# Performance work log

Measured on AMD Instinct MI355X. Metric: run time of the kernel, lower is better.

## Reference

```python
import jax, jax.numpy as jnp
import numpy as np

B, D, N, L, H, T = 256, 768, 256, 2, 8, 20
HD = D // H

def _ln(x, g, b):
    m = x.mean(-1, keepdims=True)
    v = ((x - m) ** 2).mean(-1, keepdims=True)
    return (x - m) / jnp.sqrt(v + 1e-5) * g + b

def setup_inputs() -> dict:
    key = jax.random.key(0)
    ks = jax.random.split(key, 8)
    kk = jax.random.split(ks[7], 10)
    def w(k, shape):
        return jax.random.normal(k, shape, jnp.float32) * 0.02
    return {
        'feats': jax.random.normal(ks[0], (B, D, N), jnp.float32),
        'past': jax.random.normal(ks[1], (B, 16, 6), jnp.float32),
        'w_qinit': w(ks[2], (121, D)), 'b_qinit': jnp.zeros((D,), jnp.float32),
        'pos_enc': w(ks[3], (1, N, D)),
        'w_pp': w(ks[4], (2, D)), 'b_pp': jnp.zeros((D,), jnp.float32),
        'g_pp': jnp.ones((D,), jnp.float32), 'be_pp': jnp.zeros((D,), jnp.float32),
        'time_emb': w(ks[5], (T, D)),
        'Wq': w(kk[0], (L, D, D)), 'bq': jnp.zeros((L, D), jnp.float32),
        'Wk': w(kk[1], (L, D, D)), 'bk': jnp.zeros((L, D), jnp.float32),
        'Wv': w(kk[2], (L, D, D)), 'bv': jnp.zeros((L, D), jnp.float32),
        'Wo': w(kk[3], (L, D, D)), 'bo': jnp.zeros((L, D), jnp.float32),
        'ln1_g': jnp.ones((L, D), jnp.float32), 'ln1_b': jnp.zeros((L, D), jnp.float32),
        'W1': w(kk[4], (L, D, 4 * D)), 'b1': jnp.zeros((L, 4 * D), jnp.float32),
        'W2': w(kk[5], (L, 4 * D, D)), 'b2': jnp.zeros((L, D), jnp.float32),
        'ln2_g': jnp.ones((L, D), jnp.float32), 'ln2_b': jnp.zeros((L, D), jnp.float32),
        'w_dec1': w(kk[6], (D, D)), 'b_dec1': jnp.zeros((D,), jnp.float32),
        'w_dec2': w(kk[7], (D, 2)), 'b_dec2': jnp.zeros((2,), jnp.float32),
        'intent': jax.random.randint(ks[6], (B,), 0, 3),
    }

def reference(feats, past, w_qinit, b_qinit, pos_enc, w_pp, b_pp, g_pp, be_pp,
              time_emb, Wq, bq, Wk, bk, Wv, bv, Wo, bo, ln1_g, ln1_b,
              W1, b1, W2, b2, ln2_g, ln2_b, w_dec1, b_dec1, w_dec2, b_dec2, intent):
    # tokens: [B, N, D]
    tokens = jnp.transpose(feats, (0, 2, 1)) + pos_enc
    onehot = jax.nn.one_hot(jnp.clip(intent - 1, 0, 2), 3, dtype=tokens.dtype)
    past_flat = past.reshape(B, -1)
    pad = jnp.zeros((B, 22), tokens.dtype)
    context = jnp.concatenate([onehot, past_flat, pad], axis=1) @ w_qinit + b_qinit  # [B, D]
    # precompute cross-attention K/V once per layer (tokens are constant across steps)
    Kh = (jnp.einsum('bnd,lde->lbne', tokens, Wk) + bk[:, None, None, :]).reshape(L, B, N, H, HD)
    Vh = (jnp.einsum('bnd,lde->lbne', tokens, Wv) + bv[:, None, None, :]).reshape(L, B, N, H, HD)
    scale = 1.0 / np.sqrt(HD)

    def step(carry, te):
        ctx, cp = carry
        pq = jax.nn.relu(_ln(cp @ w_pp + b_pp, g_pp, be_pp))
        x = (ctx + pq + te)[:, None, :]  # [B, 1, D]
        for l in range(L):
            q = (_ln(x, ln1_g[l], ln1_b[l]) @ Wq[l] + bq[l]).reshape(B, 1, H, HD)
            s = jnp.einsum('bqhd,bnhd->bhqn', q, Kh[l]) * scale
            a = jax.nn.softmax(s, axis=-1)
            o = jnp.einsum('bhqn,bnhd->bqhd', a, Vh[l]).reshape(B, 1, D) @ Wo[l] + bo[l]
            x = x + o
            h = jax.nn.gelu(_ln(x, ln2_g[l], ln2_b[l]) @ W1[l] + b1[l], approximate=False) @ W2[l] + b2[l]
            x = x + h
        ctx = x[:, 0]
        delta = jax.nn.gelu(ctx @ w_dec1 + b_dec1, approximate=False) @ w_dec2 + b_dec2
        cp = cp + delta
        return (ctx, cp), cp

    init = (context, past[:, -1, 0:2])
    _, ys = jax.lax.scan(step, init, time_emb)  # ys: [T, B, 2]
    return jnp.transpose(ys, (1, 0, 2))
```

## Files before the change

kernel.cpp:

```cpp
#include <hip/hip_runtime.h>
#include <hip/hip_bf16.h>
#include <math.h>

#define B_ 256
#define D_ 768
#define N_ 256
#define L_ 2
#define H_ 8
#define T_ 20
#define HD_ 96
#define D4_ 3072

typedef float f32x4v __attribute__((ext_vector_type(4)));
typedef __bf16 bf16x8v __attribute__((ext_vector_type(8)));

union V16 { uint4 u; bf16x8v v; };

__device__ __forceinline__ ushort f2b(float f) {
    union { float f; unsigned u; } x{f};
    unsigned r = x.u + 0x7fffu + ((x.u >> 16) & 1u);
    return (ushort)(r >> 16);
}
__device__ __forceinline__ float b2f(ushort s) {
    union { unsigned u; float f; } x{(unsigned)s << 16};
    return x.f;
}
__device__ __forceinline__ float gelu_f(float v) {
    return 0.5f * v * (1.0f + erff(v * 0.7071067811865476f));
}
__device__ __forceinline__ float dot8(const float* __restrict__ xp, uint4 u) {
    return xp[0] * b2f((ushort)(u.x & 0xffffu)) + xp[1] * b2f((ushort)(u.x >> 16))
         + xp[2] * b2f((ushort)(u.y & 0xffffu)) + xp[3] * b2f((ushort)(u.y >> 16))
         + xp[4] * b2f((ushort)(u.z & 0xffffu)) + xp[5] * b2f((ushort)(u.z >> 16))
         + xp[6] * b2f((ushort)(u.w & 0xffffu)) + xp[7] * b2f((ushort)(u.w >> 16));
}
__device__ __forceinline__ float blockSum(float v, float* red, int tid) {
    for (int off = 32; off; off >>= 1) v += __shfl_down(v, off, 64);
    int w = tid >> 6, lane = tid & 63;
    if (lane == 0) red[w] = v;
    __syncthreads();
    float r = red[0] + red[1] + red[2] + red[3];
    __syncthreads();
    return r;
}
__device__ __forceinline__ void gl_lds16(const ushort* g, ushort* l) {
    __builtin_amdgcn_global_load_lds((const __attribute__((address_space(1))) unsigned int*)g,
                                     (__attribute__((address_space(3))) unsigned int*)l,
                                     16, 0, 0);
}

__global__ __launch_bounds__(256) void context_kernel(const float* __restrict__ past,
                                                      const float* __restrict__ w_qinit,
                                                      const float* __restrict__ b_qinit,
                                                      const int* __restrict__ intent,
                                                      const float* __restrict__ w_pp,
                                                      const float* __restrict__ b_pp,
                                                      const float* __restrict__ g_pp,
                                                      const float* __restrict__ be_pp,
                                                      const float* __restrict__ te0,
                                                      float* __restrict__ x,
                                                      float* __restrict__ cp) {
    int b = blockIdx.x, tid = threadIdx.x;
    __shared__ float ps[96];
    __shared__ int oidx;
    __shared__ float red[4];
    if (tid < 96) ps[tid] = past[b * 96 + tid];
    if (tid == 0) {
        int iv = intent[b] - 1;
        oidx = iv < 0 ? 0 : (iv > 2 ? 2 : iv);
    }
    __syncthreads();
    float ctx[3];
    #pragma unroll
    for (int r = 0; r < 3; ++r) {
        int d = tid + r * 256;
        float acc = w_qinit[oidx * D_ + d] + b_qinit[d];
        #pragma unroll 8
        for (int p = 0; p < 96; ++p) acc += ps[p] * w_qinit[(3 + p) * D_ + d];
        ctx[r] = acc;
    }
    float c0 = ps[90], c1 = ps[91];
    if (tid == 0) { cp[b * 2] = c0; cp[b * 2 + 1] = c1; }
    float t[3];
    float s = 0, ss = 0;
    #pragma unroll
    for (int r = 0; r < 3; ++r) {
        int d = tid + r * 256;
        t[r] = c0 * w_pp[d] + c1 * w_pp[D_ + d] + b_pp[d];
        s += t[r]; ss += t[r] * t[r];
    }
    s = blockSum(s, red, tid);
    ss = blockSum(ss, red, tid);
    float mean = s * (1.0f / D_);
    float var = ss * (1.0f / D_) - mean * mean;
    float rinv = rsqrtf(var + 1e-5f);
    #pragma unroll
    for (int r = 0; r < 3; ++r) {
        int d = tid + r * 256;
        float pq = fmaxf((t[r] - mean) * rinv * g_pp[d] + be_pp[d], 0.0f);
        x[b * D_ + d] = ctx[r] + pq + te0[d];
    }
}

__global__ __launch_bounds__(256) void token_prep(const float* __restrict__ feats,
                                                  const float* __restrict__ pos_enc,
                                                  ushort* __restrict__ tokens) {
    int b = blockIdx.z;
    int d0 = blockIdx.x * 64, n0 = blockIdx.y * 64;
    __shared__ float tile[64][65];
    int tid = threadIdx.x;
    int nl = tid & 63, dl0 = tid >> 6;
    const float* fb = feats + ((size_t)b * D_ + d0) * N_ + n0;
    #pragma unroll
    for (int i = 0; i < 16; ++i) {
        int dl = dl0 + i * 4;
        tile[dl][nl] = fb[(size_t)dl * N_ + nl];
    }
    __syncthreads();
    int dq = (tid & 15) * 4;
    int ng = tid >> 4;
    #pragma unroll
    for (int i = 0; i < 4; ++i) {
        int nl2 = ng + i * 16;
        int n = n0 + nl2;
        float4 p = *(const float4*)(pos_enc + (size_t)n * D_ + d0 + dq);
        ushort4 o;
        o.x = f2b(tile[dq + 0][nl2] + p.x);
        o.y = f2b(tile[dq + 1][nl2] + p.y);
        o.z = f2b(tile[dq + 2][nl2] + p.z);
        o.w = f2b(tile[dq + 3][nl2] + p.w);
        *(ushort4*)&tokens[((size_t)b * N_ + n) * D_ + d0 + dq] = o;
    }
}

__global__ __launch_bounds__(256) void transpose_w(const float* __restrict__ W,
                                                   ushort* __restrict__ out,
                                                   const float* __restrict__ scale,
                                                   int K, int N) {
    __shared__ float t[32][33];
    int k0 = blockIdx.y * 32, n0 = blockIdx.x * 32;
    int tx = threadIdx.x & 31, ty = threadIdx.x >> 5;
    #pragma unroll
    for (int i = 0; i < 4; ++i)
        t[ty + i * 8][tx] = W[(size_t)(k0 + ty + i * 8) * N + n0 + tx];
    __syncthreads();
    #pragma unroll
    for (int i = 0; i < 4; ++i) {
        int n = n0 + ty + i * 8, k = k0 + tx;
        float v = t[tx][ty + i * 8];
        if (scale) v *= scale[k];
        out[(size_t)n * K + k] = f2b(v);
    }
}

__global__ __launch_bounds__(256) void bias_eff_kernel(const float* __restrict__ W,
                                                       const float* __restrict__ bias,
                                                       const float* __restrict__ lb,
                                                       float* __restrict__ be, int Nc) {
    int n = blockIdx.x * 256 + threadIdx.x;
    float a = bias[n];
    for (int k = 0; k < D_; ++k) a += lb[k] * W[(size_t)k * Nc + n];
    be[n] = a;
}

__global__ void kvbias_prep(const float* __restrict__ bk, const float* __restrict__ bv,
                            float* __restrict__ bc) {
    int i = blockIdx.x * 256 + threadIdx.x;
    int mi = i / D_, c = i % D_;
    int l = mi >> 1;
    bc[i] = (mi & 1 ? bv : bk)[l * D_ + c];
}

__global__ __launch_bounds__(256) void kv_gemm_mfma(const ushort* __restrict__ tokens,
                                                    const ushort* __restrict__ Wkvt,
                                                    const float* __restrict__ bias_kv,
                                                    ushort* __restrict__ Kt,
                                                    ushort* __restrict__ Vt) {
    int e0 = blockIdx.x * 128;
    int mi = e0 / D_;
    int ein = e0 % D_;
    int l = mi >> 1, isV = mi & 1;
    int m0 = blockIdx.y * 128;
    int b = m0 >> 8, ntok0 = m0 & 255;
    __shared__ __align__(16) ushort smem[17408];
    int tid = threadIdx.x;
    int w = tid >> 6, lane = tid & 63, quad = lane >> 4, l16 = lane & 15;
    int wr = w >> 1, wc = w & 1;
    f32x4v acc[4][4];
    #pragma unroll
    for (int i = 0; i < 4; ++i)
        #pragma unroll
        for (int j = 0; j < 4; ++j) acc[i][j] = (f32x4v)(0.0f);

    auto stage = [&](int buf, int k0) {
        ushort* Ab = smem + buf * 8192;
        ushort* Bb = Ab + 4096;
        #pragma unroll
        for (int vv = 0; vv < 2; ++vv) {
            int v = tid + vv * 256;
            int row = v >> 2, kq = v & 3;
            gl_lds16(&tokens[(size_t)(m0 + row) * D_ + k0 + kq * 8], Ab + w * 512 + vv * 2048);
            gl_lds16(&Wkvt[(size_t)(e0 + row) * D_ + k0 + kq * 8],   Bb + w * 512 + vv * 2048);
        }
    };

    stage(0, 0);
    asm volatile("s_waitcnt vmcnt(0)" ::: "memory");
    __syncthreads();
    int cur = 0;
    for (int k0 = 0; k0 < D_; k0 += 32) {
        if (k0 + 32 < D_) stage(cur ^ 1, k0 + 32);
        const ushort* Ab = smem + cur * 8192;
        const ushort* Bb = Ab + 4096;
        V16 a[4], bb[4];
        #pragma unroll
        for (int i = 0; i < 4; ++i)
            a[i].u = *(const uint4*)&Ab[(wr * 64 + i * 16 + l16) * 32 + quad * 8];
        #pragma unroll
        for (int j = 0; j < 4; ++j)
            bb[j].u = *(const uint4*)&Bb[(wc * 64 + j * 16 + l16) * 32 + quad * 8];
        #pragma unroll
        for (int i = 0; i < 4; ++i)
            #pragma unroll
            for (int j = 0; j < 4; ++j)
                acc[i][j] = __builtin_amdgcn_mfma_f32_16x16x32_bf16(a[i].v, bb[j].v, acc[i][j], 0, 0, 0);
        asm volatile("s_waitcnt vmcnt(0)" ::: "memory");
        __syncthreads();
        cur ^= 1;
    }

    float bcol[4];
    #pragma unroll
    for (int j = 0; j < 4; ++j)
        bcol[j] = bias_kv[e0 + wc * 64 + j * 16 + l16];

    ushort* Ct = smem;
    ushort* outbuf = isV ? Vt : Kt;
    #pragma unroll
    for (int i = 0; i < 4; ++i)
        #pragma unroll
        for (int j = 0; j < 4; ++j) {
            int e_l = wc * 64 + j * 16 + l16;
            int m_b = wr * 64 + i * 16 + quad * 4;
            ushort4 p;
            p.x = f2b(acc[i][j][0] + bcol[j]);
            p.y = f2b(acc[i][j][1] + bcol[j]);
            p.z = f2b(acc[i][j][2] + bcol[j]);
            p.w = f2b(acc[i][j][3] + bcol[j]);
            *(ushort4*)&Ct[e_l * 136 + m_b] = p;
        }
    __syncthreads();
    int e_l = tid >> 1, half = tid & 1;
    int c = ein + e_l;
    int h = c / HD_, hd = c % HD_;
    size_t dst = ((((size_t)l * B_ + b) * H_ + h) * HD_ + hd) * N_ + ntok0 + half * 64;
    #pragma unroll
    for (int p8 = 0; p8 < 8; ++p8)
        *(uint4*)&outbuf[dst + p8 * 8] = *(const uint4*)&Ct[e_l * 136 + half * 64 + p8 * 8];
}

template<int AVAR, int OMODE, int STATS, int KSPLIT>
__global__ __launch_bounds__(256) void gemm_s(const void* __restrict__ Av,
                                              const ushort* __restrict__ Bt,
                                              const float* __restrict__ bias,
                                              void* __restrict__ Cv,
                                              int K, int Nc) {
    __shared__ __align__(16) ushort As[2][2048];
    __shared__ __align__(16) ushort Bs[2][2048];
    __shared__ float smst[64][2];
    int tid = threadIdx.x;
    int m0 = blockIdx.y * 64, e0 = blockIdx.x * 64;
    int kslice = K / KSPLIT;
    int kbeg = blockIdx.z * kslice, kend = kbeg + kslice;
    int w = tid >> 6, lane = tid & 63, quad = lane >> 4, l16 = lane & 15;

    if (STATS) {
        int row = tid >> 2, part = tid & 3;
        const float* xr = (const float*)Av + (size_t)(m0 + row) * K + part * 192;
        float s = 0, ss = 0;
        #pragma unroll 4
        for (int i = 0; i < 192; i += 4) {
            float4 f = *(const float4*)(xr + i);
            s += f.x + f.y + f.z + f.w;
            ss += f.x * f.x + f.y * f.y + f.z * f.z + f.w * f.w;
        }
        s += __shfl_xor(s, 1, 64);  s += __shfl_xor(s, 2, 64);
        ss += __shfl_xor(ss, 1, 64); ss += __shfl_xor(ss, 2, 64);
        if (part == 0) {
            float mean = s * (1.0f / 768.0f);
            float var = ss * (1.0f / 768.0f) - mean * mean;
            smst[row][0] = mean;
            smst[row][1] = rsqrtf(var + 1e-5f);
        }
        __syncthreads();
    }

    bool doA = w < 2;
    int t2 = tid & 127;
    f32x4v acc[4];
    #pragma unroll
    for (int i = 0; i < 4; ++i) acc[i] = (f32x4v)(0.0f);

    auto fetchA1 = [&](int kk, int vv) -> uint4 {
        int v = t2 + vv * 128;
        int row = v >> 2, kq = v & 3;
        const float* Af = (const float*)Av + (size_t)(m0 + row) * K + kk + kq * 8;
        float4 f0 = *(const float4*)Af;
        float4 f1 = *(const float4*)(Af + 4);
        float mn = smst[row][0], rs = smst[row][1];
        f0.x = (f0.x - mn) * rs; f0.y = (f0.y - mn) * rs;
        f0.z = (f0.z - mn) * rs; f0.w = (f0.w - mn) * rs;
        f1.x = (f1.x - mn) * rs; f1.y = (f1.y - mn) * rs;
        f1.z = (f1.z - mn) * rs; f1.w = (f1.w - mn) * rs;
        uint4 u;
        u.x = (unsigned)f2b(f0.x) | ((unsigned)f2b(f0.y) << 16);
        u.y = (unsigned)f2b(f0.z) | ((unsigned)f2b(f0.w) << 16);
        u.z = (unsigned)f2b(f1.x) | ((unsigned)f2b(f1.y) << 16);
        u.w = (unsigned)f2b(f1.z) | ((unsigned)f2b(f1.w) << 16);
        return u;
    };
    auto stashA = [&](int buf, int vv, uint4 u) {
        int v = t2 + vv * 128;
        int row = v >> 2, kq = v & 3;
        *(uint4*)&As[buf][row * 32 + kq * 8] = u;
    };
    auto stageA0 = [&](int buf, int kk) {
        #pragma unroll
        for (int vv = 0; vv < 2; ++vv) {
            int v = t2 + vv * 128;
            int row = v >> 2, kq = v & 3;
            gl_lds16((const ushort*)Av + (size_t)(m0 + row) * K + kk + kq * 8,
                     &As[buf][w * 512 + vv * 1024]);
        }
    };
    auto stageB = [&](int buf, int kk) {
        int wb = w - 2;
        #pragma unroll
        for (int vv = 0; vv < 2; ++vv) {
            int v = t2 + vv * 128;
            int row = v >> 2, kq = v & 3;
            gl_lds16(&Bt[(size_t)(e0 + row) * K + kk + kq * 8],
                     &Bs[buf][wb * 512 + vv * 1024]);
        }
    };
    auto compute = [&](int buf) {
        V16 bb;
        bb.u = *(const uint4*)&Bs[buf][(w * 16 + l16) * 32 + quad * 8];
        #pragma unroll
        for (int i = 0; i < 4; ++i) {
            V16 a;
            a.u = *(const uint4*)&As[buf][(i * 16 + l16) * 32 + quad * 8];
            acc[i] = __builtin_amdgcn_mfma_f32_16x16x32_bf16(a.v, bb.v, acc[i], 0, 0, 0);
        }
    };

    if (doA) {
        if (AVAR == 0) {
            stageA0(0, kbeg);
        } else {
            uint4 p0 = fetchA1(kbeg, 0), p1 = fetchA1(kbeg, 1);
            stashA(0, 0, p0); stashA(0, 1, p1);
        }
    } else {
        stageB(0, kbeg);
    }
    asm volatile("s_waitcnt vmcnt(0)" ::: "memory");
    __syncthreads();
    int cur = 0;
    for (int kk = kbeg + 32; kk < kend; kk += 32) {
        uint4 p0, p1;
        if (doA) {
            if (AVAR == 0) stageA0(cur ^ 1, kk);
            else { p0 = fetchA1(kk, 0); p1 = fetchA1(kk, 1); }
        } else {
            stageB(cur ^ 1, kk);
        }
        compute(cur);
        if (AVAR == 1 && doA) { stashA(cur ^ 1, 0, p0); stashA(cur ^ 1, 1, p1); }
        asm volatile("s_waitcnt vmcnt(0)" ::: "memory");
        __syncthreads();
        cur ^= 1;
    }
    compute(cur);

    int n = e0 + w * 16 + l16;
    float bn = 0.0f;
    if (OMODE != 2 || blockIdx.z == 0) bn = bias[n];
    #pragma unroll
    for (int i = 0; i < 4; ++i) {
        #pragma unroll
        for (int r = 0; r < 4; ++r) {
            int m = m0 + i * 16 + quad * 4 + r;
            float v = acc[i][r] + bn;
            if (OMODE == 1) v = gelu_f(v);
            if (OMODE == 2) atomicAdd((float*)Cv + (size_t)m * Nc + n, v);
            else            ((ushort*)Cv)[(size_t)m * Nc + n] = f2b(v);
        }
    }
}

__global__ __launch_bounds__(256) void attn_fused(const float* __restrict__ x,
                                                  const ushort* __restrict__ Wqt,
                                                  const float* __restrict__ bqe,
                                                  const ushort* __restrict__ Kt,
                                                  const ushort* __restrict__ Vt,
                                                  ushort* __restrict__ att) {
    int b = blockIdx.y, h = blockIdx.x, tid = threadIdx.x;
    int w = tid >> 6, lane = tid & 63;
    __shared__ float xs[768];
    __shared__ float red[4];
    __shared__ float qs[96];
    __shared__ float spart[4][256];
    __shared__ float sc[256];
    __shared__ float opo[96];

    if (tid < 192) *(float4*)&xs[tid * 4] = *(const float4*)&x[(size_t)b * D_ + tid * 4];
    __syncthreads();

    float s = 0, ss = 0;
    #pragma unroll
    for (int r = 0; r < 3; ++r) { float v = xs[tid + r * 256]; s += v; ss += v * v; }
    s = blockSum(s, red, tid);
    ss = blockSum(ss, red, tid);
    float mean = s * (1.0f / D_);
    float var = ss * (1.0f / D_) - mean * mean;
    float rinv = rsqrtf(var + 1e-5f);
    #pragma unroll
    for (int r = 0; r < 3; ++r) { int d = tid + r * 256; xs[d] = (xs[d] - mean) * rinv; }
    __syncthreads();

    if (tid < 192) {
        int j = tid >> 1, kh = tid & 1;
        const ushort* wr = Wqt + (size_t)(h * HD_ + j) * D_ + kh * 384;
        const float* xp = xs + kh * 384;
        float acc = 0.0f;
        #pragma unroll 4
        for (int k = 0; k < 384; k += 8)
            acc += dot8(xp + k, *(const uint4*)&wr[k]);
        acc += __shfl_xor(acc, 1, 64);
        if (kh == 0) qs[j] = (acc + bqe[h * HD_ + j]) * 0.10206207261596575f;
    }
    __syncthreads();

    {
        int r2 = lane >> 5, tg = lane & 31;
        const ushort* Kp = Kt + (size_t)(b * H_ + h) * HD_ * N_;
        float s8[8];
        #pragma unroll
        for (int j = 0; j < 8; ++j) s8[j] = 0.0f;
        #pragma unroll 4
        for (int i = 0; i < 12; ++i) {
            int hd = w * 24 + i * 2 + r2;
            uint4 kk = *(const uint4*)&Kp[hd * N_ + tg * 8];
            float qv = qs[hd];
            s8[0] += qv * b2f((ushort)(kk.x & 0xffffu));
            s8[1] += qv * b2f((ushort)(kk.x >> 16));
            s8[2] += qv * b2f((ushort)(kk.y & 0xffffu));
            s8[3] += qv * b2f((ushort)(kk.y >> 16));
            s8[4] += qv * b2f((ushort)(kk.z & 0xffffu));
            s8[5] += qv * b2f((ushort)(kk.z >> 16));
            s8[6] += qv * b2f((ushort)(kk.w & 0xffffu));
            s8[7] += qv * b2f((ushort)(kk.w >> 16));
        }
        #pragma unroll
        for (int j = 0; j < 8; ++j) s8[j] += __shfl_xor(s8[j], 32, 64);
        if (r2 == 0) {
            float4 lo, hi;
            lo.x = s8[0]; lo.y = s8[1]; lo.z = s8[2]; lo.w = s8[3];
            hi.x = s8[4]; hi.y = s8[5]; hi.z = s8[6]; hi.w = s8[7];
            *(float4*)&spart[w][tg * 8] = lo;
            *(float4*)&spart[w][tg * 8 + 4] = hi;
        }
    }
    __syncthreads();

    float sv = spart[0][tid] + spart[1][tid] + spart[2][tid] + spart[3][tid];
    float m = sv;
    for (int off = 32; off; off >>= 1) m = fmaxf(m, __shfl_xor(m, off, 64));
    if (lane == 0) red[w] = m;
    __syncthreads();
    m = fmaxf(fmaxf(red[0], red[1]), fmaxf(red[2], red[3]));
    __syncthreads();
    float e = expf(sv - m);
    float tot = blockSum(e, red, tid);
    sc[tid] = e / tot;
    __syncthreads();

    if (tid < 192) {
        int hd = tid >> 1, nh = tid & 1;
        const ushort* Vr = Vt + (size_t)(b * H_ + h) * HD_ * N_ + hd * N_ + nh * 128;
        const float* scp = sc + nh * 128;
        float o = 0.0f;
        #pragma unroll 4
        for (int i = 0; i < 16; ++i)
            o += dot8(scp + i * 8, *(const uint4*)&Vr[i * 8]);
        o += __shfl_xor(o, 1, 64);
        if (nh == 0) opo[hd] = o;
    }
    __syncthreads();
    if (tid < 96) att[(size_t)b * D_ + h * HD_ + tid] = f2b(opo[tid]);
}

__global__ __launch_bounds__(256) void tail_kernel(float* __restrict__ x,
                                                   const ushort* __restrict__ dec1t,
                                                   const float* __restrict__ b_dec1,
                                                   const float* __restrict__ w_dec2,
                                                   const float* __restrict__ b_dec2,
                                                   float* __restrict__ cp,
                                                   float* __restrict__ out,
                                                   const float* __restrict__ time_emb,
                                                   const float* __restrict__ w_pp,
                                                   const float* __restrict__ b_pp,
                                                   const float* __restrict__ g_pp,
                                                   const float* __restrict__ be_pp,
                                                   int t) {
    int b = blockIdx.x, tid = threadIdx.x;
    __shared__ float xs[768];
    __shared__ float red[4];
    #pragma unroll
    for (int r = 0; r < 3; ++r) xs[tid + r * 256] = x[b * D_ + tid + r * 256];
    __syncthreads();
    float d0 = 0, d1 = 0, d2 = 0;
    const ushort* w0 = dec1t + (size_t)tid * D_;
    const ushort* w1 = w0 + (size_t)256 * D_;
    const ushort* w2 = w0 + (size_t)512 * D_;
    #pragma unroll 2
    for (int k = 0; k < 768; k += 8) {
        d0 += dot8(xs + k, *(const uint4*)&w0[k]);
        d1 += dot8(xs + k, *(const uint4*)&w1[k]);
        d2 += dot8(xs + k, *(const uint4*)&w2[k]);
    }
    float v0 = gelu_f(d0 + b_dec1[tid]);
    float v1 = gelu_f(d1 + b_dec1[tid + 256]);
    float v2 = gelu_f(d2 + b_dec1[tid + 512]);
    float p0 = v0 * w_dec2[tid * 2]     + v1 * w_dec2[(tid + 256) * 2]     + v2 * w_dec2[(tid + 512) * 2];
    float p1 = v0 * w_dec2[tid * 2 + 1] + v1 * w_dec2[(tid + 256) * 2 + 1] + v2 * w_dec2[(tid + 512) * 2 + 1];
    p0 = blockSum(p0, red, tid);
    p1 = blockSum(p1, red, tid);
    float c0 = cp[b * 2] + p0 + b_dec2[0];
    float c1 = cp[b * 2 + 1] + p1 + b_dec2[1];
    if (tid == 0) {
        cp[b * 2] = c0;
        cp[b * 2 + 1] = c1;
        out[(b * T_ + t) * 2] = c0;
        out[(b * T_ + t) * 2 + 1] = c1;
    }
    if (t < T_ - 1) {
        const float* te = time_emb + (size_t)(t + 1) * D_;
        float tv[3];
        float s = 0, ss = 0;
        #pragma unroll
        for (int r = 0; r < 3; ++r) {
            int d = tid + r * 256;
            tv[r] = c0 * w_pp[d] + c1 * w_pp[D_ + d] + b_pp[d];
            s += tv[r]; ss += tv[r] * tv[r];
        }
        s = blockSum(s, red, tid);
        ss = blockSum(ss, red, tid);
        float mean = s * (1.0f / D_);
        float var = ss * (1.0f / D_) - mean * mean;
        float rinv = rsqrtf(var + 1e-5f);
        #pragma unroll
        for (int r = 0; r < 3; ++r) {
            int d = tid + r * 256;
            float pq = fmaxf((tv[r] - mean) * rinv * g_pp[d] + be_pp[d], 0.0f);
            x[b * D_ + d] += pq + te[d];
        }
    }
}

extern "C" void kernel_launch(void* const* d_in, const int* in_sizes, int n_in,
                              void* d_out, int out_size, void* d_ws, size_t ws_size,
                              hipStream_t stream) {
    const float* feats   = (const float*)d_in[0];
    const float* past    = (const float*)d_in[1];
    const float* w_qinit = (const float*)d_in[2];
    const float* b_qinit = (const float*)d_in[3];
    const float* pos_enc = (const float*)d_in[4];
    const float* w_pp    = (const float*)d_in[5];
    const float* b_pp    = (const float*)d_in[6];
    const float* g_pp    = (const float*)d_in[7];
    const float* be_pp   = (const float*)d_in[8];
    const float* time_emb= (const float*)d_in[9];
    const float* Wq      = (const float*)d_in[10];
    const float* bq      = (const float*)d_in[11];
    const float* Wk      = (const float*)d_in[12];
    const float* bk      = (const float*)d_in[13];
    const float* Wv      = (const float*)d_in[14];
    const float* bv      = (const float*)d_in[15];
    const float* Wo      = (const float*)d_in[16];
    const float* bo      = (const float*)d_in[17];
    const float* ln1_g   = (const float*)d_in[18];
    const float* ln1_b   = (const float*)d_in[19];
    const float* W1      = (const float*)d_in[20];
    const float* b1      = (const float*)d_in[21];
    const float* W2      = (const float*)d_in[22];
    const float* b2      = (const float*)d_in[23];
    const float* ln2_g   = (const float*)d_in[24];
    const float* ln2_b   = (const float*)d_in[25];
    const float* w_dec1  = (const float*)d_in[26];
    const float* b_dec1  = (const float*)d_in[27];
    const float* w_dec2  = (const float*)d_in[28];
    const float* b_dec2  = (const float*)d_in[29];
    const int*   intent  = (const int*)d_in[30];
    float* out = (float*)d_out;

    const size_t WD = (size_t)D_ * D_;
    const size_t WD4 = (size_t)D_ * D4_;
    const size_t kv_elems = (size_t)L_ * B_ * H_ * HD_ * N_;
    const size_t kv_l = (size_t)B_ * H_ * HD_ * N_;

    char* wp = (char*)d_ws;
    ushort* Kt     = (ushort*)wp; wp += kv_elems * 2;
    ushort* Vt     = (ushort*)wp; wp += kv_elems * 2;
    ushort* tokens = (ushort*)wp; wp += (size_t)B_ * N_ * D_ * 2;
    ushort* Wkvt   = (ushort*)wp; wp += 4 * WD * 2;
    ushort* Wqt    = (ushort*)wp; wp += 2 * WD * 2;
    ushort* Wot    = (ushort*)wp; wp += 2 * WD * 2;
    ushort* W1t    = (ushort*)wp; wp += 2 * WD4 * 2;
    ushort* W2t    = (ushort*)wp; wp += 2 * WD4 * 2;
    ushort* dec1t  = (ushort*)wp; wp += WD * 2;
    float* bias_kv = (float*)wp;  wp += 4 * D_ * 4;
    float* bqe     = (float*)wp;  wp += 2 * D_ * 4;
    float* b1e     = (float*)wp;  wp += 2 * D4_ * 4;
    float* x       = (float*)wp;  wp += (size_t)B_ * D_ * 4;
    ushort* attbuf = (ushort*)wp; wp += (size_t)B_ * D_ * 2;
    ushort* h1     = (ushort*)wp; wp += (size_t)B_ * D4_ * 2;
    float* cp      = (float*)wp;  wp += (size_t)B_ * 2 * 4;

    context_kernel<<<B_, 256, 0, stream>>>(past, w_qinit, b_qinit, intent,
                                           w_pp, b_pp, g_pp, be_pp, time_emb, x, cp);
    token_prep<<<dim3(12, 4, 256), 256, 0, stream>>>(feats, pos_enc, tokens);
    kvbias_prep<<<12, 256, 0, stream>>>(bk, bv, bias_kv);
    for (int l = 0; l < L_; ++l) {
        transpose_w<<<dim3(24, 24), 256, 0, stream>>>(Wk + l * WD, Wkvt + (2 * l + 0) * WD, nullptr, D_, D_);
        transpose_w<<<dim3(24, 24), 256, 0, stream>>>(Wv + l * WD, Wkvt + (2 * l + 1) * WD, nullptr, D_, D_);
        transpose_w<<<dim3(24, 24), 256, 0, stream>>>(Wq + l * WD, Wqt + l * WD, ln1_g + l * D_, D_, D_);
        transpose_w<<<dim3(24, 24), 256, 0, stream>>>(Wo + l * WD, Wot + l * WD, nullptr, D_, D_);
        transpose_w<<<dim3(96, 24), 256, 0, stream>>>(W1 + l * WD4, W1t + l * WD4, ln2_g + l * D_, D_, D4_);
        transpose_w<<<dim3(24, 96), 256, 0, stream>>>(W2 + l * WD4, W2t + l * WD4, nullptr, D4_, D_);
        bias_eff_kernel<<<3, 256, 0, stream>>>(Wq + l * WD, bq + l * D_, ln1_b + l * D_, bqe + l * D_, D_);
        bias_eff_kernel<<<12, 256, 0, stream>>>(W1 + l * WD4, b1 + l * D4_, ln2_b + l * D_, b1e + l * D4_, D4_);
    }
    transpose_w<<<dim3(24, 24), 256, 0, stream>>>(w_dec1, dec1t, nullptr, D_, D_);

    kv_gemm_mfma<<<dim3(24, 512), 256, 0, stream>>>(tokens, Wkvt, bias_kv, Kt, Vt);

    for (int t = 0; t < T_; ++t) {
        for (int l = 0; l < L_; ++l) {
            attn_fused<<<dim3(H_, B_), 256, 0, stream>>>(x, Wqt + l * WD, bqe + l * D_,
                                                         Kt + l * kv_l, Vt + l * kv_l, attbuf);
            gemm_s<0, 2, 0, 4><<<dim3(12, 4, 4), 256, 0, stream>>>(attbuf, Wot + l * WD,
                                                                   bo + l * D_, x, D_, D_);
            gemm_s<1, 1, 1, 1><<<dim3(48, 4), 256, 0, stream>>>(x, W1t + l * WD4,
                                                                b1e + l * D4_, h1, D_, D4_);
            gemm_s<0, 2, 0, 4><<<dim3(12, 4, 4), 256, 0, stream>>>(h1, W2t + l * WD4,
                                                                   b2 + l * D_, x, D4_, D_);
        }
        tail_kernel<<<B_, 256, 0, stream>>>(x, dec1t, b_dec1, w_dec2, b_dec2, cp, out,
                                            time_emb, w_pp, b_pp, g_pp, be_pp, t);
    }
}
```

Before: 6.781 ms.

## Swizzle LDS tiles, remap KV GEMM block order, parallelize bias fold

Applies an XOR swizzle to the k-chunk position within each 32-wide LDS row in both the KV GEMM and gemm_s, on both the global-to-LDS staging and the MFMA operand reads, to reduce LDS bank conflicts. The KV GEMM launch becomes a 1D grid with a remapped block order, so that concurrently running blocks share token rows and weight tiles in cache. The bias-folding kernel now splits the K reduction across four wavefronts and stages the LN bias in shared memory, raising parallelism from 3/12 blocks to 12/48. The risk is an indexing mismatch between the swizzled writes and reads, which would give wrong results.

```diff
diff --git a/kernel.cpp b/kernel.cpp
--- a/kernel.cpp
+++ b/kernel.cpp
@@ -157,10 +157,22 @@
                                                        const float* __restrict__ bias,
                                                        const float* __restrict__ lb,
                                                        float* __restrict__ be, int Nc) {
-    int n = blockIdx.x * 256 + threadIdx.x;
-    float a = bias[n];
-    for (int k = 0; k < D_; ++k) a += lb[k] * W[(size_t)k * Nc + n];
-    be[n] = a;
+    __shared__ float lbs[768];
+    __shared__ float part[4][64];
+    int tid = threadIdx.x;
+    for (int i = tid; i < 768; i += 256) lbs[i] = lb[i];
+    __syncthreads();
+    int n0 = blockIdx.x * 64;
+    int nl = tid & 63, kp = tid >> 6;
+    int n = n0 + nl;
+    float a = 0.0f;
+    #pragma unroll 4
+    for (int k = kp * 192; k < kp * 192 + 192; ++k)
+        a += lbs[k] * W[(size_t)k * Nc + n];
+    part[kp][nl] = a;
+    __syncthreads();
+    if (tid < 64)
+        be[n0 + tid] = bias[n0 + tid] + part[0][tid] + part[1][tid] + part[2][tid] + part[3][tid];
 }
 
 __global__ void kvbias_prep(const float* __restrict__ bk, const float* __restrict__ bv,
@@ -176,16 +188,21 @@
                                                     const float* __restrict__ bias_kv,
                                                     ushort* __restrict__ Kt,
                                                     ushort* __restrict__ Vt) {
-    int e0 = blockIdx.x * 128;
+    int bid = blockIdx.x;
+    int swb = (bid & 7) * 1536 + (bid >> 3);
+    int e_tile = swb % 24, m_tile = swb / 24;
+    int e0 = e_tile * 128;
     int mi = e0 / D_;
     int ein = e0 % D_;
     int l = mi >> 1, isV = mi & 1;
-    int m0 = blockIdx.y * 128;
+    int m0 = m_tile * 128;
     int b = m0 >> 8, ntok0 = m0 & 255;
     __shared__ __align__(16) ushort smem[17408];
     int tid = threadIdx.x;
     int w = tid >> 6, lane = tid & 63, quad = lane >> 4, l16 = lane & 15;
     int wr = w >> 1, wc = w & 1;
+    int swz = (l16 >> 1) & 3;
+    int rchunk = ((quad ^ swz) & 3) * 8;
     f32x4v acc[4][4];
     #pragma unroll
     for (int i = 0; i < 4; ++i)
@@ -198,7 +215,8 @@
         #pragma unroll
         for (int vv = 0; vv < 2; ++vv) {
             int v = tid + vv * 256;
-            int row = v >> 2, kq = v & 3;
+            int row = v >> 2;
+            int kq = (v & 3) ^ ((row >> 1) & 3);
             gl_lds16(&tokens[(size_t)(m0 + row) * D_ + k0 + kq * 8], Ab + w * 512 + vv * 2048);
             gl_lds16(&Wkvt[(size_t)(e0 + row) * D_ + k0 + kq * 8],   Bb + w * 512 + vv * 2048);
         }
@@ -215,10 +233,10 @@
         V16 a[4], bb[4];
         #pragma unroll
         for (int i = 0; i < 4; ++i)
-            a[i].u = *(const uint4*)&Ab[(wr * 64 + i * 16 + l16) * 32 + quad * 8];
+            a[i].u = *(const uint4*)&Ab[(wr * 64 + i * 16 + l16) * 32 + rchunk];
         #pragma unroll
         for (int j = 0; j < 4; ++j)
-            bb[j].u = *(const uint4*)&Bb[(wc * 64 + j * 16 + l16) * 32 + quad * 8];
+            bb[j].u = *(const uint4*)&Bb[(wc * 64 + j * 16 + l16) * 32 + rchunk];
         #pragma unroll
         for (int i = 0; i < 4; ++i)
             #pragma unroll
@@ -273,6 +291,8 @@
     int kslice = K / KSPLIT;
     int kbeg = blockIdx.z * kslice, kend = kbeg + kslice;
     int w = tid >> 6, lane = tid & 63, quad = lane >> 4, l16 = lane & 15;
+    int swz = (l16 >> 1) & 3;
+    int rchunk = ((quad ^ swz) & 3) * 8;
 
     if (STATS) {
         int row = tid >> 2, part = tid & 3;
@@ -322,13 +342,14 @@
     auto stashA = [&](int buf, int vv, uint4 u) {
         int v = t2 + vv * 128;
         int row = v >> 2, kq = v & 3;
-        *(uint4*)&As[buf][row * 32 + kq * 8] = u;
+        *(uint4*)&As[buf][row * 32 + ((kq ^ ((row >> 1) & 3)) & 3) * 8] = u;
     };
     auto stageA0 = [&](int buf, int kk) {
         #pragma unroll
         for (int vv = 0; vv < 2; ++vv) {
             int v = t2 + vv * 128;
-            int row = v >> 2, kq = v & 3;
+            int row = v >> 2;
+            int kq = (v & 3) ^ ((row >> 1) & 3);
             gl_lds16((const ushort*)Av + (size_t)(m0 + row) * K + kk + kq * 8,
                      &As[buf][w * 512 + vv * 1024]);
         }
@@ -338,18 +359,19 @@
         #pragma unroll
         for (int vv = 0; vv < 2; ++vv) {
             int v = t2 + vv * 128;
-            int row = v >> 2, kq = v & 3;
+            int row = v >> 2;
+            int kq = (v & 3) ^ ((row >> 1) & 3);
             gl_lds16(&Bt[(size_t)(e0 + row) * K + kk + kq * 8],
                      &Bs[buf][wb * 512 + vv * 1024]);
         }
     };
     auto compute = [&](int buf) {
         V16 bb;
-        bb.u = *(const uint4*)&Bs[buf][(w * 16 + l16) * 32 + quad * 8];
+        bb.u = *(const uint4*)&Bs[buf][(w * 16 + l16) * 32 + rchunk];
         #pragma unroll
         for (int i = 0; i < 4; ++i) {
             V16 a;
-            a.u = *(const uint4*)&As[buf][(i * 16 + l16) * 32 + quad * 8];
+            a.u = *(const uint4*)&As[buf][(i * 16 + l16) * 32 + rchunk];
             acc[i] = __builtin_amdgcn_mfma_f32_16x16x32_bf16(a.v, bb.v, acc[i], 0, 0, 0);
         }
     };
@@ -639,12 +661,12 @@
         transpose_w<<<dim3(24, 24), 256, 0, stream>>>(Wo + l * WD, Wot + l * WD, nullptr, D_, D_);
         transpose_w<<<dim3(96, 24), 256, 0, stream>>>(W1 + l * WD4, W1t + l * WD4, ln2_g + l * D_, D_, D4_);
         transpose_w<<<dim3(24, 96), 256, 0, stream>>>(W2 + l * WD4, W2t + l * WD4, nullptr, D4_, D_);
-        bias_eff_kernel<<<3, 256, 0, stream>>>(Wq + l * WD, bq + l * D_, ln1_b + l * D_, bqe + l * D_, D_);
-        bias_eff_kernel<<<12, 256, 0, stream>>>(W1 + l * WD4, b1 + l * D4_, ln2_b + l * D_, b1e + l * D4_, D4_);
+        bias_eff_kernel<<<12, 256, 0, stream>>>(Wq + l * WD, bq + l * D_, ln1_b + l * D_, bqe + l * D_, D_);
+        bias_eff_kernel<<<48, 256, 0, stream>>>(W1 + l * WD4, b1 + l * D4_, ln2_b + l * D_, b1e + l * D4_, D4_);
     }
     transpose_w<<<dim3(24, 24), 256, 0, stream>>>(w_dec1, dec1t, nullptr, D_, D_);
 
-    kv_gemm_mfma<<<dim3(24, 512), 256, 0, stream>>>(tokens, Wkvt, bias_kv, Kt, Vt);
+    kv_gemm_mfma<<<12288, 256, 0, stream>>>(tokens, Wkvt, bias_kv, Kt, Vt);
 
     for (int t = 0; t < T_; ++t) {
         for (int l = 0; l < L_; ++l) {
```

New measurement: 6.806 ms. No clear change (+0.4%).
